# Kernel optimization log

Measured on AMD Instinct MI355X. Metric: run time of the kernel, lower is better.

Reference implementation:

```python
import jax, jax.numpy as jnp
import numpy as np

B, N, H, R = 128, 512, 256, 3
VIRTUAL_DECAY = 0.7


def _build_tree():
    # Deterministic random recursive tree: parent[i] ~ U[0, i)
    rng = np.random.default_rng(0)
    parent = np.zeros(N, np.int64)
    for i in range(1, N):
        parent[i] = rng.integers(0, i)
    depth = np.zeros(N, np.int64)
    for i in range(1, N):
        depth[i] = depth[parent[i]] + 1
    rel_edge = rng.integers(0, R, N)          # relation type of edge (parent -> i)
    virtual = rng.random(N) < 0.1
    children = [[] for _ in range(N)]
    for i in range(1, N):
        children[parent[i]].append(i)
    # Group internal nodes by depth (deepest first == valid post-order batching),
    # pad ragged child lists per level.
    levels = []
    for d in range(int(depth.max()), -1, -1):
        nodes = [n for n in range(N) if depth[n] == d and len(children[n]) > 0]
        if not nodes:
            continue
        cmax = max(len(children[n]) for n in nodes)
        M = len(nodes)
        cidx = np.zeros((M, cmax), np.int64)
        cmask = np.zeros((M, cmax), np.float32)
        crel = np.zeros((M, cmax), np.int64)
        cvirt = np.zeros((M, cmax), bool)
        for m, n in enumerate(nodes):
            ch = children[n]
            k = len(ch)
            cidx[m, :k] = ch
            cmask[m, :k] = 1.0
            crel[m, :k] = rel_edge[ch]
            cvirt[m, :k] = virtual[ch]
        levels.append((jnp.array(nodes), jnp.array(cidx), jnp.array(cmask),
                       jnp.array(crel), jnp.array(cvirt)))
    return levels

LEVELS = _build_tree()


def _forward(node_features, W_enc, b_enc, rel_emb, W_i, b_i, W_o, b_o, W_u, b_u,
             W_f, b_f, w_attn, b_attn):
    h = node_features @ W_enc + b_enc            # (B, N, H) node_encoder
    c = jnp.zeros_like(h)
    for node_ids, cidx, cmask, crel, cvirt in LEVELS:
        x = h[:, node_ids]                       # (B, M, H) input_vec (== encoded feats)
        ch_h = h[:, cidx]                        # (B, M, C, H)
        ch_c = c[:, cidx]
        # virtual-node decay + padding mask
        decay = jnp.where(cvirt, VIRTUAL_DECAY, 1.0).astype(h.dtype) * cmask  # (M, C)
        ch_h = ch_h * decay[None, :, :, None]
        ch_c = ch_c * decay[None, :, :, None]
        # relation-aware attention over children
        re = rel_emb[crel]                       # (M, C, H)
        scores = jnp.einsum('bmch,h->bmc', re[None] + ch_h, w_attn) + b_attn[0]
        scores = jnp.where(cmask[None] > 0, scores, -1e9)
        attw = jax.nn.softmax(scores, axis=-1)   # (B, M, C)
        h_sum = jnp.einsum('bmc,bmch->bmh', attw, ch_h)
        # per-relation forget transform (note: original applies NO sigmoid here)
        f = jnp.zeros_like(ch_h)
        for r in range(R):
            fr = jnp.einsum('bmch,hk->bmck', ch_h, W_f[r]) + b_f[r]
            f = f + fr * (crel == r).astype(h.dtype)[None, :, :, None]
        c_sum = jnp.sum(f * ch_c, axis=2)        # (B, M, H); padded ch_c is 0
        comb = jnp.concatenate([x, h_sum], axis=-1)  # (B, M, 2H)
        i_g = jax.nn.sigmoid(comb @ W_i + b_i)
        o_g = jax.nn.sigmoid(comb @ W_o + b_o)
        u_g = jnp.tanh(comb @ W_u + b_u)
        c_new = i_g * u_g + c_sum
        h_new = o_g * jnp.tanh(c_new)
        h = h.at[:, node_ids].set(h_new)
        c = c.at[:, node_ids].set(c_new)
    return h[:, 0]                               # pooling == 'root' (root = 0)


def setup_inputs() -> dict:
    key = jax.random.key(0)
    ks = jax.random.split(key, 8)
    s = 0.05
    f32 = jnp.float32
    return {
        'node_features': jax.random.normal(ks[0], (B, N, H), f32),
        'W_enc': jax.random.normal(ks[1], (H, H), f32) * s,
        'b_enc': jnp.full((H,), 0.1, f32),
        'rel_emb': jax.random.normal(ks[2], (R, H), f32) * s,
        'W_i': jax.random.normal(ks[3], (2 * H, H), f32) * s,
        'b_i': jnp.full((H,), 0.1, f32),
        'W_o': jax.random.normal(ks[4], (2 * H, H), f32) * s,
        'b_o': jnp.full((H,), 0.1, f32),
        'W_u': jax.random.normal(ks[5], (2 * H, H), f32) * s,
        'b_u': jnp.full((H,), 0.1, f32),
        'W_f': jax.random.normal(ks[6], (R, H, H), f32) * s,
        'b_f': jnp.full((R, H), 0.1, f32),
        'w_attn': jax.random.normal(ks[7], (H,), f32) * s,
        'b_attn': jnp.full((1,), 0.1, f32),
    }


def reference(node_features, W_enc, b_enc, rel_emb, W_i, b_i, W_o, b_o, W_u, b_u,
              W_f, b_f, w_attn, b_attn):
    return _forward(node_features, W_enc, b_enc, rel_emb, W_i, b_i, W_o, b_o,
                    W_u, b_u, W_f, b_f, w_attn, b_attn)
```

## Files before the change

### kernel.cpp

```cpp
#include <hip/hip_runtime.h>
#include <stdint.h>
#include <string.h>
#include <math.h>

#define NB 128
#define NN 512
#define NH 256
#define NR 3
#define TH_TINY 24

typedef __attribute__((ext_vector_type(8))) short bh8;
typedef __attribute__((ext_vector_type(4))) float f32x4;

struct Pcg {
  __uint128_t state, inc;
  bool has32; uint32_t buf32;
};

static const __uint128_t PCG_MULT =
    (((__uint128_t)2549297995355413924ULL) << 64) | 4865540595714422341ULL;

static inline uint64_t pcg_next64(Pcg& s) {
  s.state = s.state * PCG_MULT + s.inc;
  uint64_t hi = (uint64_t)(s.state >> 64), lo = (uint64_t)s.state;
  uint64_t x = hi ^ lo;
  unsigned rot = (unsigned)(s.state >> 122) & 63u;
  return (x >> rot) | (x << ((64u - rot) & 63u));
}
static inline uint32_t pcg_next32(Pcg& s) {
  if (s.has32) { s.has32 = false; return s.buf32; }
  uint64_t n = pcg_next64(s);
  s.has32 = true; s.buf32 = (uint32_t)(n >> 32);
  return (uint32_t)n;
}
static inline uint64_t pcg_bounded(Pcg& s, uint64_t high) {
  uint64_t rng = high - 1;
  if (rng == 0) return 0;
  uint32_t rng_excl = (uint32_t)rng + 1u;
  uint64_t m = (uint64_t)pcg_next32(s) * (uint64_t)rng_excl;
  uint32_t leftover = (uint32_t)m;
  if (leftover < rng_excl) {
    uint32_t threshold = (uint32_t)((0xFFFFFFFFu - (uint32_t)rng) % rng_excl);
    while (leftover < threshold) {
      m = (uint64_t)pcg_next32(s) * (uint64_t)rng_excl;
      leftover = (uint32_t)m;
    }
  }
  return m >> 32;
}
static inline double pcg_double(Pcg& s) {
  return (double)(pcg_next64(s) >> 11) * (1.0 / 9007199254740992.0);
}

static void pcg_seed0(Pcg& s) {
  uint32_t pool[4];
  uint32_t hc = 0x43b0d7e5u;
  auto hashmix = [&hc](uint32_t v) -> uint32_t {
    v ^= hc; hc *= 0x931e8875u; v *= hc; v ^= v >> 16; return v;
  };
  auto mix = [](uint32_t x, uint32_t y) -> uint32_t {
    uint32_t r = 0xca01f9ddu * x - 0x4973f715u * y; r ^= r >> 16; return r;
  };
  for (int i = 0; i < 4; i++) pool[i] = hashmix(0u);
  for (int src = 0; src < 4; src++)
    for (int dst = 0; dst < 4; dst++)
      if (src != dst) pool[dst] = mix(pool[dst], hashmix(pool[src]));
  uint32_t gs[8]; uint32_t hb = 0x8b51f9ddu;
  for (int i = 0; i < 8; i++) {
    uint32_t dv = pool[i & 3];
    dv ^= hb; hb *= 0x58f38dedu; dv *= hb; dv ^= dv >> 16;
    gs[i] = dv;
  }
  uint64_t w0 = (uint64_t)gs[0] | ((uint64_t)gs[1] << 32);
  uint64_t w1 = (uint64_t)gs[2] | ((uint64_t)gs[3] << 32);
  uint64_t w2 = (uint64_t)gs[4] | ((uint64_t)gs[5] << 32);
  uint64_t w3 = (uint64_t)gs[6] | ((uint64_t)gs[7] << 32);
  __uint128_t initstate = (((__uint128_t)w0) << 64) | w1;
  __uint128_t initseq   = (((__uint128_t)w2) << 64) | w3;
  s.state = 0;
  s.inc = (initseq << 1) | 1;
  s.state = s.state * PCG_MULT + s.inc;
  s.state += initstate;
  s.state = s.state * PCG_MULT + s.inc;
  s.has32 = false; s.buf32 = 0;
}

struct TreeMeta {
  int nodes[512];
  int cstart[512];
  int ccount[512];
  int echild[512];
  int erel[512];
  float edecay[512];
  int cechild[512];
  int cerel[512];
  float cedec[512];
  int cens[513];
};
struct HostTree {
  TreeMeta meta;
  int n_levels;
  int level_off[520];
  int level_M[520];
};

static void build_tree_host(HostTree& T) {
  Pcg st; pcg_seed0(st);
  int parent[NN], depth[NN], rel[NN];
  unsigned char virt[NN];
  parent[0] = 0; depth[0] = 0;
  for (int i = 1; i < NN; i++) parent[i] = (int)pcg_bounded(st, (uint64_t)i);
  for (int i = 1; i < NN; i++) depth[i] = depth[parent[i]] + 1;
  for (int i = 0; i < NN; i++) rel[i] = (int)pcg_bounded(st, (uint64_t)NR);
  for (int i = 0; i < NN; i++) virt[i] = (pcg_double(st) < 0.1) ? 1 : 0;

  int childcnt[NN]; memset(childcnt, 0, sizeof(childcnt));
  for (int i = 1; i < NN; i++) childcnt[parent[i]]++;
  int maxd = 0;
  for (int i = 0; i < NN; i++) if (depth[i] > maxd) maxd = depth[i];

  int ni = 0, ne = 0, nec = 0;
  T.n_levels = 0;
  for (int d = maxd; d >= 0; d--) {
    int mstart = ni;
    for (int n = 0; n < NN; n++) {
      if (depth[n] == d && childcnt[n] > 0) {
        T.meta.nodes[ni] = n;
        T.meta.cstart[ni] = ne;
        T.meta.ccount[ni] = childcnt[n];
        T.meta.cens[ni] = nec;
        for (int i2 = 1; i2 < NN; i2++) {
          if (parent[i2] == n) {
            T.meta.echild[ne] = i2;
            T.meta.erel[ne] = rel[i2];
            T.meta.edecay[ne] = virt[i2] ? 0.7f : 1.0f;
            ne++;
            if (childcnt[i2] > 0) {
              T.meta.cechild[nec] = i2;
              T.meta.cerel[nec] = rel[i2];
              T.meta.cedec[nec] = virt[i2] ? 0.7f : 1.0f;
              nec++;
            }
          }
        }
        ni++;
      }
    }
    if (ni > mstart) {
      T.level_off[T.n_levels] = mstart;
      T.level_M[T.n_levels] = ni - mstart;
      T.n_levels++;
    }
  }
  T.meta.cens[ni] = nec;
}

__device__ __forceinline__ uint16_t f2bf(float f) {
  uint32_t u = __float_as_uint(f);
  return (uint16_t)((u + 0x7fffu + ((u >> 16) & 1u)) >> 16);
}
__device__ __forceinline__ float bf2f(uint16_t b) {
  return __uint_as_float(((uint32_t)b) << 16);
}
__device__ __forceinline__ float sigm(float x) {
  return 1.f / (1.f + expf(-x));
}

__device__ __forceinline__ void stage_bf16(uint16_t* __restrict__ sm,
    const uint16_t* __restrict__ src, int stride, int rows) {
  const int chunks = rows << 3;
  for (int cch = threadIdx.x; cch < chunks; cch += 256) {
    const int row = cch >> 3, k = (cch & 7) << 3;
    uint4 v = *(const uint4*)(src + (size_t)row * stride + k);
    *(uint4*)(sm + (((row << 6) + k) ^ ((row & 7) << 3))) = v;
  }
}
__device__ __forceinline__ void stage_f32(uint16_t* __restrict__ sm,
    const float* __restrict__ src, int stride, int rows) {
  const int chunks = rows << 3;
  for (int cch = threadIdx.x; cch < chunks; cch += 256) {
    const int row = cch >> 3, k = (cch & 7) << 3;
    const float* p = src + (size_t)row * stride + k;
    float4 a = *(const float4*)p, b = *(const float4*)(p + 4);
    uint4 w;
    w.x = (uint32_t)f2bf(a.x) | ((uint32_t)f2bf(a.y) << 16);
    w.y = (uint32_t)f2bf(a.z) | ((uint32_t)f2bf(a.w) << 16);
    w.z = (uint32_t)f2bf(b.x) | ((uint32_t)f2bf(b.y) << 16);
    w.w = (uint32_t)f2bf(b.z) | ((uint32_t)f2bf(b.w) << 16);
    *(uint4*)(sm + (((row << 6) + k) ^ ((row & 7) << 3))) = w;
  }
}
__device__ __forceinline__ bh8 fld(const uint16_t* __restrict__ sm, int row, int k) {
  return *(const bh8*)(sm + (((row << 6) + k) ^ ((row & 7) << 3)));
}

#define LDROW(BUF, CH) do { \
    const uint4* p_ = (const uint4*)(hbase + (size_t)(CH) * NH); \
    BUF[0]=p_[0]; BUF[1]=p_[1]; BUF[2]=p_[2]; BUF[3]=p_[3]; \
    BUF[4]=p_[4]; BUF[5]=p_[5]; BUF[6]=p_[6]; BUF[7]=p_[7]; } while (0)
#define ACCROW(BUF, W) do { const float w_ = (W); \
    _Pragma("unroll") for (int v_ = 0; v_ < 8; v_++) { \
      const uint16_t* pe_ = (const uint16_t*)&BUF[v_]; \
      _Pragma("unroll") for (int q_ = 0; q_ < 8; q_++) \
        hs[v_*8+q_] = fmaf(bf2f(pe_[q_]), w_, hs[v_*8+q_]); } } while (0)

__global__ __launch_bounds__(256) void k_prep(const float* __restrict__ We,
    const float* __restrict__ Wf, const float* __restrict__ Wi,
    const float* __restrict__ Wo, const float* __restrict__ Wu,
    uint16_t* __restrict__ WeT, uint16_t* __restrict__ WfT,
    uint16_t* __restrict__ WgT) {
  const int i = blockIdx.x * 256 + threadIdx.x;
  if (i < 65536) {
    const int n = i >> 8, k = i & 255;
    WeT[i] = f2bf(We[k * 256 + n]);
  }
  const int i2 = i - 65536;
  if (i2 >= 0 && i2 < 196608) {
    const int r = i2 >> 16, rem = i2 & 65535, n = rem >> 8, k = rem & 255;
    WfT[i2] = f2bf(Wf[r * 65536 + k * 256 + n]);
  }
  const int i3 = i - 262144;
  if (i3 >= 0 && i3 < 393216) {
    const int g = i3 >> 17, rem = i3 & 131071, n = rem >> 9, k = rem & 511;
    const float* S = (g == 0) ? Wi : (g == 1) ? Wo : Wu;
    WgT[i3] = f2bf(S[k * 256 + n]);
  }
}

__global__ __launch_bounds__(256) void k_enc(const float* __restrict__ nf,
    const uint16_t* __restrict__ WeT, const float* __restrict__ b_enc,
    uint16_t* __restrict__ h_bf, uint16_t* __restrict__ x_enc) {
  __shared__ __align__(16) uint16_t smA[128 * 64];
  __shared__ __align__(16) uint16_t smB[128 * 64];
  const int bm = blockIdx.x * 128, bn = blockIdx.y * 128;
  const int tid = threadIdx.x, wid = tid >> 6, lane = tid & 63;
  const int wr = wid >> 1, wc2 = wid & 1, lr = lane & 15, lk = (lane >> 4) << 3;
  f32x4 acc[4][4] = {};
  for (int k0 = 0; k0 < 256; k0 += 64) {
    __syncthreads();
    stage_f32(smA, nf + (size_t)bm * NH + k0, NH, 128);
    stage_bf16(smB, WeT + (size_t)bn * 256 + k0, 256, 128);
    __syncthreads();
#pragma unroll
    for (int ks = 0; ks < 2; ks++) {
      bh8 af[4], bfr[4];
#pragma unroll
      for (int i = 0; i < 4; i++) af[i] = fld(smA, wr * 64 + i * 16 + lr, ks * 32 + lk);
#pragma unroll
      for (int j = 0; j < 4; j++) bfr[j] = fld(smB, wc2 * 64 + j * 16 + lr, ks * 32 + lk);
#pragma unroll
      for (int i = 0; i < 4; i++)
#pragma unroll
        for (int j = 0; j < 4; j++)
          acc[i][j] = __builtin_amdgcn_mfma_f32_16x16x32_bf16(af[i], bfr[j], acc[i][j], 0, 0, 0);
    }
  }
#pragma unroll
  for (int i = 0; i < 4; i++) {
#pragma unroll
    for (int j = 0; j < 4; j++) {
      const int col = bn + wc2 * 64 + j * 16 + (lane & 15);
      const float be = b_enc[col];
#pragma unroll
      for (int r = 0; r < 4; r++) {
        const int row = bm + wr * 64 + i * 16 + (lane >> 4) * 4 + r;
        const uint16_t hv = f2bf(acc[i][j][r] + be);
        h_bf[(size_t)row * NH + col] = hv;
        x_enc[(size_t)row * NH + col] = hv;
      }
    }
  }
}

__global__ __launch_bounds__(256) void k_sv0(const uint16_t* __restrict__ h_bf,
    const float* __restrict__ w_attn, float* __restrict__ svp) {
  const int idx = blockIdx.x * 256 + threadIdx.x;
  const int g = idx & 15;
  const size_t row = (size_t)(idx >> 4);
  const uint16_t* hp = h_bf + row * NH + g * 16;
  uint4 p0 = *(const uint4*)hp, p1 = *(const uint4*)(hp + 8);
  const uint16_t* e0 = (const uint16_t*)&p0;
  const uint16_t* e1 = (const uint16_t*)&p1;
  float s = 0.f;
#pragma unroll
  for (int u = 0; u < 8; u++) s = fmaf(bf2f(e0[u]), w_attn[g * 16 + u], s);
#pragma unroll
  for (int u = 0; u < 8; u++) s = fmaf(bf2f(e1[u]), w_attn[g * 16 + 8 + u], s);
  svp[idx] = s;
}

__global__ __launch_bounds__(256) void k_lvl(
    uint16_t* h_bf, float* c, float* __restrict__ svp,
    const uint16_t* __restrict__ x_enc,
    const uint16_t* __restrict__ WfT, const uint16_t* __restrict__ WgT,
    const float* __restrict__ b_f, const float* __restrict__ b_i,
    const float* __restrict__ b_o, const float* __restrict__ b_u,
    const float* __restrict__ rel_emb, const float* __restrict__ w_attn,
    const float* __restrict__ b_attn, float* __restrict__ out,
    const TreeMeta* __restrict__ tm, int nb) {
  __shared__ float sc[64 * 65];
  __shared__ float swa[256];
  __shared__ float sRE[3];
  __shared__ int chl[64]; __shared__ int rll[64]; __shared__ float dcl[64];
  __shared__ __align__(16) uint16_t hsum[4 * 4096];

  const int bx = blockIdx.x, mloc = bx >> 1, b0 = (bx & 1) * 64;
  const int cslice = blockIdx.y * 64;
  const int gi = nb + mloc;
  const int nd = tm->nodes[gi], cs = tm->cstart[gi], cc = tm->ccount[gi];
  const int ce0 = tm->cens[gi], nic = tm->cens[gi + 1] - ce0;
  const int tid = threadIdx.x, wid = tid >> 6, lane = tid & 63;
  const int lr2 = lane & 15, hi4 = (lane >> 4), lk = hi4 << 3;
  const int colw = cslice + wid * 16 + lr2;

  if (tid < cc) {
    chl[tid] = tm->echild[cs + tid];
    rll[tid] = tm->erel[cs + tid];
    dcl[tid] = tm->edecay[cs + tid];
  }
  swa[tid] = w_attn[tid];
  if (wid < 3) {
    float p = 0.f;
#pragma unroll
    for (int i = 0; i < 4; i++) p += rel_emb[wid * NH + lane + 64 * i] * w_attn[lane + 64 * i];
#pragma unroll
    for (int off = 32; off; off >>= 1) p += __shfl_down(p, off);
    if (lane == 0) sRE[wid] = p;
  }
  __syncthreads();

  const float ba = b_attn[0];
  if (tid < 64) {
    const float* svpb = svp + (size_t)(b0 + tid) * NN * 16;
    for (int e = 0; e < cc; e++) {
      const float4* p = (const float4*)(svpb + chl[e] * 16);
      float4 a = p[0], b2 = p[1], c2 = p[2], d2 = p[3];
      float s = ((a.x + a.y) + (a.z + a.w)) + ((b2.x + b2.y) + (b2.z + b2.w)) +
                ((c2.x + c2.y) + (c2.z + c2.w)) + ((d2.x + d2.y) + (d2.z + d2.w));
      sc[tid * 65 + e] = sRE[rll[e]] + dcl[e] * s + ba;
    }
    float mx = -1e30f;
    for (int e = 0; e < cc; e++) mx = fmaxf(mx, sc[tid * 65 + e]);
    float ss = 0.f;
    for (int e = 0; e < cc; e++) ss += expf(sc[tid * 65 + e] - mx);
    const float inv = 1.0f / ss;
    for (int e = 0; e < cc; e++) sc[tid * 65 + e] = expf(sc[tid * 65 + e] - mx) * inv * dcl[e];
  }
  __syncthreads();

  const int sb = tid >> 2, sq = tid & 3;
  {
    float hs[64];
#pragma unroll
    for (int v = 0; v < 64; v++) hs[v] = 0.f;
    const uint16_t* hbase = h_bf + (size_t)(b0 + sb) * NN * NH + sq * 64;
    uint4 bufA[8], bufB[8];
    LDROW(bufA, chl[0]);
    int e = 0;
    for (; e + 2 <= cc; e += 2) {
      LDROW(bufB, chl[e + 1]);
      ACCROW(bufA, sc[sb * 65 + e]);
      if (e + 2 < cc) LDROW(bufA, chl[e + 2]);
      ACCROW(bufB, sc[sb * 65 + e + 1]);
    }
    if (e < cc) ACCROW(bufA, sc[sb * 65 + e]);
    uint16_t* sub = hsum + sq * 4096;
#pragma unroll
    for (int v = 0; v < 32; v++) {
      uint32_t pk = (uint32_t)f2bf(hs[2 * v]) | ((uint32_t)f2bf(hs[2 * v + 1]) << 16);
      const int elem = ((sb << 6) + 2 * v) ^ ((sb & 7) << 3);
      *(uint32_t*)(sub + elem) = pk;
    }
  }

  f32x4 csum[4] = {};
#pragma unroll 2
  for (int e = 0; e < nic; e++) {
    const int ch = tm->cechild[ce0 + e];
    const int rel = tm->cerel[ce0 + e];
    const float dec = tm->cedec[ce0 + e];
    const uint16_t* Wr = WfT + (size_t)rel * 65536 + (size_t)colw * 256;
    f32x4 facc[4] = {};
#pragma unroll
    for (int k0 = 0; k0 < 8; k0++) {
      const int kk = k0 * 32 + lk;
      bh8 af[4];
#pragma unroll
      for (int i = 0; i < 4; i++)
        af[i] = *(const bh8*)(h_bf + ((size_t)(b0 + i * 16 + lr2) * NN + ch) * NH + kk);
      const bh8 bq = *(const bh8*)(Wr + kk);
#pragma unroll
      for (int i = 0; i < 4; i++)
        facc[i] = __builtin_amdgcn_mfma_f32_16x16x32_bf16(af[i], bq, facc[i], 0, 0, 0);
    }
    const float bfv = b_f[rel * NH + colw];
#pragma unroll
    for (int i = 0; i < 4; i++) {
#pragma unroll
      for (int r = 0; r < 4; r++) {
        const int brow = b0 + i * 16 + hi4 * 4 + r;
        const float cch = c[((size_t)brow * NN + ch) * NH + colw];
        csum[i][r] += (dec * facc[i][r] + bfv) * (dec * cch);
      }
    }
  }
  __syncthreads();

  f32x4 ga[3][4] = {};
#pragma unroll
  for (int k32 = 0; k32 < 16; k32++) {
    const int kk = k32 * 32 + lk;
    bh8 af[4], bq[3];
    if (k32 < 8) {
#pragma unroll
      for (int i = 0; i < 4; i++)
        af[i] = *(const bh8*)(x_enc + ((size_t)(b0 + i * 16 + lr2) * NN + nd) * NH + kk);
    } else {
      const int kx = k32 - 8;
#pragma unroll
      for (int i = 0; i < 4; i++)
        af[i] = fld(hsum + (kx >> 1) * 4096, i * 16 + lr2, (kx & 1) * 32 + lk);
    }
#pragma unroll
    for (int g = 0; g < 3; g++)
      bq[g] = *(const bh8*)(WgT + ((size_t)g << 17) + (size_t)colw * 512 + kk);
#pragma unroll
    for (int g = 0; g < 3; g++)
#pragma unroll
      for (int i = 0; i < 4; i++)
        ga[g][i] = __builtin_amdgcn_mfma_f32_16x16x32_bf16(af[i], bq[g], ga[g][i], 0, 0, 0);
  }

  const float bi_ = b_i[colw], bo_ = b_o[colw], bu_ = b_u[colw];
  const float wac = swa[colw];
#pragma unroll
  for (int i = 0; i < 4; i++) {
#pragma unroll
    for (int r = 0; r < 4; r++) {
      const int brow = b0 + i * 16 + hi4 * 4 + r;
      const size_t idx = ((size_t)brow * NN + nd) * NH + colw;
      const float ig = sigm(ga[0][i][r] + bi_);
      const float og = sigm(ga[1][i][r] + bo_);
      const float ug = tanhf(ga[2][i][r] + bu_);
      const float cn = fmaf(ig, ug, csum[i][r]);
      c[idx] = cn;
      const float hn = og * tanhf(cn);
      h_bf[idx] = f2bf(hn);
      if (nd == 0) out[(size_t)brow * NH + colw] = hn;
      float pv = hn * wac;
      pv += __shfl_xor(pv, 1); pv += __shfl_xor(pv, 2);
      pv += __shfl_xor(pv, 4); pv += __shfl_xor(pv, 8);
      if (lr2 == 0) svp[((size_t)brow * NN + nd) * 16 + (cslice >> 4) + wid] = pv;
    }
  }
}

__global__ __launch_bounds__(256) void k_tiny(
    uint16_t* h_bf, float* c, float* __restrict__ svp,
    const uint16_t* __restrict__ x_enc,
    const uint16_t* __restrict__ WfT, const uint16_t* __restrict__ WgT,
    const float* __restrict__ b_f, const float* __restrict__ b_i,
    const float* __restrict__ b_o, const float* __restrict__ b_u,
    const float* __restrict__ rel_emb, const float* __restrict__ w_attn,
    const float* __restrict__ b_attn, float* __restrict__ out,
    const TreeMeta* __restrict__ tm, int nb) {
  __shared__ float sc[64 * 65];
  __shared__ float swa[256];
  __shared__ float sRE[3];
  __shared__ int chl[64]; __shared__ int rll[64]; __shared__ float dcl[64];
  __shared__ __align__(16) uint16_t hsum[4 * 4096];

  const int c0 = blockIdx.x * 16;
  const int mloc = blockIdx.y >> 1, b0 = (blockIdx.y & 1) * 64;
  const int gi = nb + mloc;
  const int nd = tm->nodes[gi], cs = tm->cstart[gi], cc = tm->ccount[gi];
  const int ce0 = tm->cens[gi], nic = tm->cens[gi + 1] - ce0;
  const int tid = threadIdx.x, wid = tid >> 6, lane = tid & 63;
  const int lb = lane & 15, lq = lane >> 4;
  const int colw = c0 + lb;
  const int wrow = b0 + wid * 16;

  if (tid < cc) {
    chl[tid] = tm->echild[cs + tid];
    rll[tid] = tm->erel[cs + tid];
    dcl[tid] = tm->edecay[cs + tid];
  }
  swa[tid] = w_attn[tid];
  if (wid < 3) {
    float p = 0.f;
#pragma unroll
    for (int i = 0; i < 4; i++) p += rel_emb[wid * NH + lane + 64 * i] * w_attn[lane + 64 * i];
#pragma unroll
    for (int off = 32; off; off >>= 1) p += __shfl_down(p, off);
    if (lane == 0) sRE[wid] = p;
  }
  __syncthreads();

  const float ba = b_attn[0];
  if (tid < 64) {
    const float* svpb = svp + (size_t)(b0 + tid) * NN * 16;
    for (int e = 0; e < cc; e++) {
      const float4* p = (const float4*)(svpb + chl[e] * 16);
      float4 a = p[0], b2 = p[1], c2 = p[2], d2 = p[3];
      float s = ((a.x + a.y) + (a.z + a.w)) + ((b2.x + b2.y) + (b2.z + b2.w)) +
                ((c2.x + c2.y) + (c2.z + c2.w)) + ((d2.x + d2.y) + (d2.z + d2.w));
      sc[tid * 65 + e] = sRE[rll[e]] + dcl[e] * s + ba;
    }
    float mx = -1e30f;
    for (int e = 0; e < cc; e++) mx = fmaxf(mx, sc[tid * 65 + e]);
    float ss = 0.f;
    for (int e = 0; e < cc; e++) ss += expf(sc[tid * 65 + e] - mx);
    const float inv = 1.0f / ss;
    for (int e = 0; e < cc; e++) sc[tid * 65 + e] = expf(sc[tid * 65 + e] - mx) * inv * dcl[e];
  }
  __syncthreads();

  const int sb = tid >> 2, sq = tid & 3;
  {
    float hs[64];
#pragma unroll
    for (int v = 0; v < 64; v++) hs[v] = 0.f;
    const uint16_t* hbase = h_bf + (size_t)(b0 + sb) * NN * NH + sq * 64;
    uint4 bufA[8], bufB[8];
    LDROW(bufA, chl[0]);
    int e = 0;
    for (; e + 2 <= cc; e += 2) {
      LDROW(bufB, chl[e + 1]);
      ACCROW(bufA, sc[sb * 65 + e]);
      if (e + 2 < cc) LDROW(bufA, chl[e + 2]);
      ACCROW(bufB, sc[sb * 65 + e + 1]);
    }
    if (e < cc) ACCROW(bufA, sc[sb * 65 + e]);
    uint16_t* sub = hsum + sq * 4096;
#pragma unroll
    for (int v = 0; v < 32; v++) {
      uint32_t pk = (uint32_t)f2bf(hs[2 * v]) | ((uint32_t)f2bf(hs[2 * v + 1]) << 16);
      const int elem = ((sb << 6) + 2 * v) ^ ((sb & 7) << 3);
      *(uint32_t*)(sub + elem) = pk;
    }
  }

  f32x4 csum = {};
#pragma unroll 2
  for (int e = 0; e < nic; e++) {
    const int ch = tm->cechild[ce0 + e];
    const int rel = tm->cerel[ce0 + e];
    const float dec = tm->cedec[ce0 + e];
    const uint16_t* Wr = WfT + (size_t)rel * 65536 + (size_t)colw * 256;
    f32x4 facc = {};
#pragma unroll
    for (int k0 = 0; k0 < 8; k0++) {
      const int kk = k0 * 32 + lq * 8;
      const bh8 af = *(const bh8*)(h_bf + ((size_t)(wrow + lb) * NN + ch) * NH + kk);
      const bh8 bq = *(const bh8*)(Wr + kk);
      facc = __builtin_amdgcn_mfma_f32_16x16x32_bf16(af, bq, facc, 0, 0, 0);
    }
    const float bfv = b_f[rel * NH + colw];
#pragma unroll
    for (int r = 0; r < 4; r++) {
      const int brow = wrow + lq * 4 + r;
      const float cch = c[((size_t)brow * NN + ch) * NH + colw];
      csum[r] += (dec * facc[r] + bfv) * (dec * cch);
    }
  }
  __syncthreads();

  f32x4 ga[3] = {};
#pragma unroll
  for (int k32 = 0; k32 < 16; k32++) {
    const int kk = k32 * 32 + lq * 8;
    bh8 af;
    if (k32 < 8) {
      af = *(const bh8*)(x_enc + ((size_t)(wrow + lb) * NN + nd) * NH + kk);
    } else {
      const int kx = k32 - 8;
      af = fld(hsum + (kx >> 1) * 4096, wid * 16 + lb, (kx & 1) * 32 + lq * 8);
    }
#pragma unroll
    for (int g = 0; g < 3; g++) {
      const bh8 bq = *(const bh8*)(WgT + ((size_t)g << 17) + (size_t)colw * 512 + kk);
      ga[g] = __builtin_amdgcn_mfma_f32_16x16x32_bf16(af, bq, ga[g], 0, 0, 0);
    }
  }

  const float bi_ = b_i[colw], bo_ = b_o[colw], bu_ = b_u[colw];
  const float wac = swa[colw];
#pragma unroll
  for (int r = 0; r < 4; r++) {
    const int brow = wrow + lq * 4 + r;
    const size_t idx = ((size_t)brow * NN + nd) * NH + colw;
    const float ig = sigm(ga[0][r] + bi_);
    const float og = sigm(ga[1][r] + bo_);
    const float ug = tanhf(ga[2][r] + bu_);
    const float cn = fmaf(ig, ug, csum[r]);
    c[idx] = cn;
    const float hn = og * tanhf(cn);
    h_bf[idx] = f2bf(hn);
    if (nd == 0) out[(size_t)brow * NH + colw] = hn;
    float pv = hn * wac;
    pv += __shfl_xor(pv, 1); pv += __shfl_xor(pv, 2);
    pv += __shfl_xor(pv, 4); pv += __shfl_xor(pv, 8);
    if (lb == 0) svp[((size_t)brow * NN + nd) * 16 + (c0 >> 4)] = pv;
  }
}

extern "C" void kernel_launch(void* const* d_in, const int* in_sizes, int n_in,
                              void* d_out, int out_size, void* d_ws, size_t ws_size,
                              hipStream_t stream) {
  (void)in_sizes; (void)n_in; (void)out_size; (void)ws_size;
  const float* nf      = (const float*)d_in[0];
  const float* W_enc   = (const float*)d_in[1];
  const float* b_enc   = (const float*)d_in[2];
  const float* rel_emb = (const float*)d_in[3];
  const float* W_i     = (const float*)d_in[4];
  const float* b_i     = (const float*)d_in[5];
  const float* W_o     = (const float*)d_in[6];
  const float* b_o     = (const float*)d_in[7];
  const float* W_u     = (const float*)d_in[8];
  const float* b_u     = (const float*)d_in[9];
  const float* W_f     = (const float*)d_in[10];
  const float* b_f     = (const float*)d_in[11];
  const float* w_attn  = (const float*)d_in[12];
  const float* b_attn  = (const float*)d_in[13];
  float* out = (float*)d_out;

  static HostTree T;
  build_tree_host(T);

  char* ws = (char*)d_ws;
  const size_t OFF_HBF = 32768;
  const size_t SZ_HBF  = (size_t)NB * NN * NH * 2;
  const size_t OFF_XE  = OFF_HBF + SZ_HBF;
  const size_t OFF_WET = OFF_XE + SZ_HBF;
  const size_t OFF_WFT = OFF_WET + 131072;
  const size_t OFF_WGT = OFF_WFT + 393216;
  const size_t OFF_C   = OFF_WGT + 786432;
  const size_t SZ_C    = (size_t)NB * NN * NH * 4;
  const size_t OFF_SVP = OFF_C + SZ_C;

  TreeMeta* dm = (TreeMeta*)ws;
  uint16_t* h_bf = (uint16_t*)(ws + OFF_HBF);
  uint16_t* x_enc = (uint16_t*)(ws + OFF_XE);
  uint16_t* WeT = (uint16_t*)(ws + OFF_WET);
  uint16_t* WfT = (uint16_t*)(ws + OFF_WFT);
  uint16_t* WgT = (uint16_t*)(ws + OFF_WGT);
  float* c = (float*)(ws + OFF_C);
  float* svp = (float*)(ws + OFF_SVP);

  hipMemcpyAsync(dm, &T.meta, sizeof(TreeMeta), hipMemcpyHostToDevice, stream);

  k_prep<<<2560, 256, 0, stream>>>(W_enc, W_f, W_i, W_o, W_u, WeT, WfT, WgT);
  k_enc<<<dim3((NB * NN) / 128, 2), 256, 0, stream>>>(nf, WeT, b_enc, h_bf, x_enc);
  k_sv0<<<dim3((NB * NN * 16) / 256), 256, 0, stream>>>(h_bf, w_attn, svp);

  for (int l = 0; l < T.n_levels; l++) {
    const int Mfull = T.level_M[l];
    if (Mfull >= TH_TINY) {
      for (int c0 = 0; c0 < Mfull; c0 += 128) {
        const int Mc = (Mfull - c0) < 128 ? (Mfull - c0) : 128;
        k_lvl<<<dim3(2 * Mc, 4), 256, 0, stream>>>(h_bf, c, svp, x_enc, WfT, WgT,
            b_f, b_i, b_o, b_u, rel_emb, w_attn, b_attn, out, dm,
            T.level_off[l] + c0);
      }
    } else {
      k_tiny<<<dim3(16, 2 * Mfull), 256, 0, stream>>>(h_bf, c, svp, x_enc, WfT, WgT,
          b_f, b_i, b_o, b_u, rel_emb, w_attn, b_attn, out, dm,
          T.level_off[l]);
    }
  }
}
```

Baseline: 612.9 us.

## Split level kernel into attention-combine and gate kernels to remove redundant work

```diff
diff --git a/kernel.cpp b/kernel.cpp
--- a/kernel.cpp
+++ b/kernel.cpp
@@ -7,7 +7,7 @@
 #define NN 512
 #define NH 256
 #define NR 3
-#define TH_TINY 24
+#define TH_SPLIT 16
 
 typedef __attribute__((ext_vector_type(8))) short bh8;
 typedef __attribute__((ext_vector_type(4))) float f32x4;
@@ -289,36 +289,24 @@
   svp[idx] = s;
 }
 
-__global__ __launch_bounds__(256) void k_lvl(
-    uint16_t* h_bf, float* c, float* __restrict__ svp,
-    const uint16_t* __restrict__ x_enc,
-    const uint16_t* __restrict__ WfT, const uint16_t* __restrict__ WgT,
-    const float* __restrict__ b_f, const float* __restrict__ b_i,
-    const float* __restrict__ b_o, const float* __restrict__ b_u,
+__global__ __launch_bounds__(256) void k_att(
+    const uint16_t* __restrict__ h_bf, const float* __restrict__ svp,
     const float* __restrict__ rel_emb, const float* __restrict__ w_attn,
-    const float* __restrict__ b_attn, float* __restrict__ out,
+    const float* __restrict__ b_attn, uint16_t* __restrict__ comb,
     const TreeMeta* __restrict__ tm, int nb) {
   __shared__ float sc[64 * 65];
-  __shared__ float swa[256];
   __shared__ float sRE[3];
   __shared__ int chl[64]; __shared__ int rll[64]; __shared__ float dcl[64];
-  __shared__ __align__(16) uint16_t hsum[4 * 4096];
-
-  const int bx = blockIdx.x, mloc = bx >> 1, b0 = (bx & 1) * 64;
-  const int cslice = blockIdx.y * 64;
+  const int mloc = blockIdx.x >> 1, b0 = (blockIdx.x & 1) * 64;
   const int gi = nb + mloc;
-  const int nd = tm->nodes[gi], cs = tm->cstart[gi], cc = tm->ccount[gi];
-  const int ce0 = tm->cens[gi], nic = tm->cens[gi + 1] - ce0;
+  const int cs = tm->cstart[gi], cc = tm->ccount[gi];
   const int tid = threadIdx.x, wid = tid >> 6, lane = tid & 63;
-  const int lr2 = lane & 15, hi4 = (lane >> 4), lk = hi4 << 3;
-  const int colw = cslice + wid * 16 + lr2;
 
   if (tid < cc) {
     chl[tid] = tm->echild[cs + tid];
     rll[tid] = tm->erel[cs + tid];
     dcl[tid] = tm->edecay[cs + tid];
   }
-  swa[tid] = w_attn[tid];
   if (wid < 3) {
     float p = 0.f;
 #pragma unroll
@@ -349,29 +337,48 @@
   __syncthreads();
 
   const int sb = tid >> 2, sq = tid & 3;
-  {
-    float hs[64];
-#pragma unroll
-    for (int v = 0; v < 64; v++) hs[v] = 0.f;
-    const uint16_t* hbase = h_bf + (size_t)(b0 + sb) * NN * NH + sq * 64;
-    uint4 bufA[8], bufB[8];
-    LDROW(bufA, chl[0]);
-    int e = 0;
-    for (; e + 2 <= cc; e += 2) {
-      LDROW(bufB, chl[e + 1]);
-      ACCROW(bufA, sc[sb * 65 + e]);
-      if (e + 2 < cc) LDROW(bufA, chl[e + 2]);
-      ACCROW(bufB, sc[sb * 65 + e + 1]);
-    }
-    if (e < cc) ACCROW(bufA, sc[sb * 65 + e]);
-    uint16_t* sub = hsum + sq * 4096;
-#pragma unroll
-    for (int v = 0; v < 32; v++) {
-      uint32_t pk = (uint32_t)f2bf(hs[2 * v]) | ((uint32_t)f2bf(hs[2 * v + 1]) << 16);
-      const int elem = ((sb << 6) + 2 * v) ^ ((sb & 7) << 3);
-      *(uint32_t*)(sub + elem) = pk;
-    }
-  }
+  float hs[64];
+#pragma unroll
+  for (int v = 0; v < 64; v++) hs[v] = 0.f;
+  const uint16_t* hbase = h_bf + (size_t)(b0 + sb) * NN * NH + sq * 64;
+  uint4 bufA[8], bufB[8];
+  LDROW(bufA, chl[0]);
+  int e = 0;
+  for (; e + 2 <= cc; e += 2) {
+    LDROW(bufB, chl[e + 1]);
+    ACCROW(bufA, sc[sb * 65 + e]);
+    if (e + 2 < cc) LDROW(bufA, chl[e + 2]);
+    ACCROW(bufB, sc[sb * 65 + e + 1]);
+  }
+  if (e < cc) ACCROW(bufA, sc[sb * 65 + e]);
+  uint16_t* cb = comb + ((size_t)(mloc * 128 + b0 + sb)) * 256 + sq * 64;
+#pragma unroll
+  for (int v = 0; v < 8; v++) {
+    uint4 w;
+    w.x = (uint32_t)f2bf(hs[8 * v + 0]) | ((uint32_t)f2bf(hs[8 * v + 1]) << 16);
+    w.y = (uint32_t)f2bf(hs[8 * v + 2]) | ((uint32_t)f2bf(hs[8 * v + 3]) << 16);
+    w.z = (uint32_t)f2bf(hs[8 * v + 4]) | ((uint32_t)f2bf(hs[8 * v + 5]) << 16);
+    w.w = (uint32_t)f2bf(hs[8 * v + 6]) | ((uint32_t)f2bf(hs[8 * v + 7]) << 16);
+    *(uint4*)(cb + v * 8) = w;
+  }
+}
+
+__global__ __launch_bounds__(256) void k_gat(
+    uint16_t* h_bf, float* c, float* __restrict__ svp,
+    const uint16_t* __restrict__ x_enc, const uint16_t* __restrict__ comb,
+    const uint16_t* __restrict__ WfT, const uint16_t* __restrict__ WgT,
+    const float* __restrict__ b_f, const float* __restrict__ b_i,
+    const float* __restrict__ b_o, const float* __restrict__ b_u,
+    const float* __restrict__ w_attn, float* __restrict__ out,
+    const TreeMeta* __restrict__ tm, int nb) {
+  const int bx = blockIdx.x, mloc = bx >> 1, b0 = (bx & 1) * 64;
+  const int cslice = blockIdx.y * 64;
+  const int gi = nb + mloc;
+  const int nd = tm->nodes[gi];
+  const int ce0 = tm->cens[gi], nic = tm->cens[gi + 1] - ce0;
+  const int tid = threadIdx.x, wid = tid >> 6, lane = tid & 63;
+  const int lr2 = lane & 15, hi4 = (lane >> 4), lk = hi4 << 3;
+  const int colw = cslice + wid * 16 + lr2;
 
   f32x4 csum[4] = {};
 #pragma unroll 2
@@ -404,7 +411,6 @@
       }
     }
   }
-  __syncthreads();
 
   f32x4 ga[3][4] = {};
 #pragma unroll
@@ -416,10 +422,9 @@
       for (int i = 0; i < 4; i++)
         af[i] = *(const bh8*)(x_enc + ((size_t)(b0 + i * 16 + lr2) * NN + nd) * NH + kk);
     } else {
-      const int kx = k32 - 8;
 #pragma unroll
       for (int i = 0; i < 4; i++)
-        af[i] = fld(hsum + (kx >> 1) * 4096, i * 16 + lr2, (kx & 1) * 32 + lk);
+        af[i] = *(const bh8*)(comb + ((size_t)(mloc * 128 + b0 + i * 16 + lr2)) * 256 + (kk - 256));
     }
 #pragma unroll
     for (int g = 0; g < 3; g++)
@@ -432,7 +437,7 @@
   }
 
   const float bi_ = b_i[colw], bo_ = b_o[colw], bu_ = b_u[colw];
-  const float wac = swa[colw];
+  const float wac = w_attn[colw];
 #pragma unroll
   for (int i = 0; i < 4; i++) {
 #pragma unroll
@@ -628,15 +633,16 @@
   build_tree_host(T);
 
   char* ws = (char*)d_ws;
-  const size_t OFF_HBF = 32768;
-  const size_t SZ_HBF  = (size_t)NB * NN * NH * 2;
-  const size_t OFF_XE  = OFF_HBF + SZ_HBF;
-  const size_t OFF_WET = OFF_XE + SZ_HBF;
-  const size_t OFF_WFT = OFF_WET + 131072;
-  const size_t OFF_WGT = OFF_WFT + 393216;
-  const size_t OFF_C   = OFF_WGT + 786432;
-  const size_t SZ_C    = (size_t)NB * NN * NH * 4;
-  const size_t OFF_SVP = OFF_C + SZ_C;
+  const size_t OFF_HBF  = 32768;
+  const size_t SZ_HBF   = (size_t)NB * NN * NH * 2;
+  const size_t OFF_XE   = OFF_HBF + SZ_HBF;
+  const size_t OFF_WET  = OFF_XE + SZ_HBF;
+  const size_t OFF_WFT  = OFF_WET + 131072;
+  const size_t OFF_WGT  = OFF_WFT + 393216;
+  const size_t OFF_C    = OFF_WGT + 786432;
+  const size_t SZ_C     = (size_t)NB * NN * NH * 4;
+  const size_t OFF_SVP  = OFF_C + SZ_C;
+  const size_t OFF_COMB = OFF_SVP + (size_t)NB * NN * 16 * 4;
 
   TreeMeta* dm = (TreeMeta*)ws;
   uint16_t* h_bf = (uint16_t*)(ws + OFF_HBF);
@@ -646,6 +652,7 @@
   uint16_t* WgT = (uint16_t*)(ws + OFF_WGT);
   float* c = (float*)(ws + OFF_C);
   float* svp = (float*)(ws + OFF_SVP);
+  uint16_t* comb = (uint16_t*)(ws + OFF_COMB);
 
   hipMemcpyAsync(dm, &T.meta, sizeof(TreeMeta), hipMemcpyHostToDevice, stream);
 
@@ -655,16 +662,18 @@
 
   for (int l = 0; l < T.n_levels; l++) {
     const int Mfull = T.level_M[l];
-    if (Mfull >= TH_TINY) {
+    if (Mfull >= TH_SPLIT) {
       for (int c0 = 0; c0 < Mfull; c0 += 128) {
         const int Mc = (Mfull - c0) < 128 ? (Mfull - c0) : 128;
-        k_lvl<<<dim3(2 * Mc, 4), 256, 0, stream>>>(h_bf, c, svp, x_enc, WfT, WgT,
-            b_f, b_i, b_o, b_u, rel_emb, w_attn, b_attn, out, dm,
-            T.level_off[l] + c0);
+        const int nb = T.level_off[l] + c0;
+        k_att<<<dim3(2 * Mc), 256, 0, stream>>>(h_bf, svp, rel_emb, w_attn,
+            b_attn, comb, dm, nb);
+        k_gat<<<dim3(2 * Mc, 4), 256, 0, stream>>>(h_bf, c, svp, x_enc, comb,
+            WfT, WgT, b_f, b_i, b_o, b_u, w_attn, out, dm, nb);
       }
     } else {
-      k_tiny<<<dim3(16, 2 * Mfull), 256, 0, stream>>>(h_bf, c, svp, x_enc, WfT, WgT,
-          b_f, b_i, b_o, b_u, rel_emb, w_attn, b_attn, out, dm,
+      k_tiny<<<dim3(16, 2 * Mfull), 256, 0, stream>>>(h_bf, c, svp, x_enc,
+          WfT, WgT, b_f, b_i, b_o, b_u, rel_emb, w_attn, b_attn, out, dm,
           T.level_off[l]);
     }
   }
```

Result: slower. 703.6 us (+14.8%).
